# Optimization experiments

Measured on AMD Instinct MI355X. Metric: run time of the kernel, lower is better.

Reference implementation:

```python
import jax, jax.numpy as jnp
import numpy as np

B, L, D_MODEL = 2, 2048, 1024
D_STATE, D_CONV, EXPAND, DT_RANK = 16, 4, 2, 64
D_INNER = EXPAND * D_MODEL


def setup_inputs() -> dict:
    key = jax.random.key(0)
    ks = jax.random.split(key, 12)
    s = 0.02
    A_log = jnp.log(jnp.broadcast_to(jnp.arange(1, D_STATE + 1, dtype=jnp.float32), (D_INNER, D_STATE)))
    return {
        "x": jax.random.normal(ks[0], (B, L, D_MODEL), jnp.float32),
        "W_in": jax.random.normal(ks[1], (2 * D_INNER, D_MODEL), jnp.float32) * s,
        "conv_w": jax.random.normal(ks[2], (D_INNER, 1, D_CONV), jnp.float32) * 0.2,
        "conv_b": jax.random.normal(ks[3], (D_INNER,), jnp.float32) * s,
        "W_xp": jax.random.normal(ks[4], (DT_RANK + 2 * D_STATE, D_INNER), jnp.float32) * s,
        "W_dt": jax.random.normal(ks[5], (D_INNER, DT_RANK), jnp.float32) * 0.1,
        "b_dt": jax.random.uniform(ks[6], (D_INNER,), jnp.float32, -4.6, -2.3),  # ~softplus^-1 of small dt
        "A_log": A_log,
        "D": jnp.ones((D_INNER,), jnp.float32),
        "W_out_ssm": jax.random.normal(ks[7], (D_MODEL, D_INNER), jnp.float32) * s,
        "W_out": jax.random.normal(ks[8], (D_MODEL, D_MODEL), jnp.float32) * s,
        "b_out": jnp.zeros((D_MODEL,), jnp.float32),
    }


def _mamba_block(x, W_in, conv_w, conv_b, W_xp, W_dt, b_dt, A_log, D, W_out_ssm, W_out, b_out):
    d_inner = conv_b.shape[0]
    d_state = A_log.shape[1]
    dt_rank = W_dt.shape[1]
    d_conv = conv_w.shape[-1]

    # in_proj -> x branch and gate z
    xz = x @ W_in.T                         # [B, L, 2*d_inner]
    xin, z = jnp.split(xz, 2, axis=-1)

    # causal depthwise conv over time
    xc = jnp.transpose(xin, (0, 2, 1))      # [B, d_inner, L]
    xc = jax.lax.conv_general_dilated(
        xc, conv_w, window_strides=(1,), padding=[(d_conv - 1, 0)],
        feature_group_count=d_inner)
    xc = jax.nn.silu(xc + conv_b[None, :, None])
    xs = jnp.transpose(xc, (0, 2, 1))       # [B, L, d_inner]

    # input-dependent dt, B, C
    x_dbl = xs @ W_xp.T                     # [B, L, dt_rank + 2*d_state]
    dt, Bm, Cm = jnp.split(x_dbl, [dt_rank, dt_rank + d_state], axis=-1)
    dt = jax.nn.softplus(dt @ W_dt.T + b_dt)  # [B, L, d_inner]

    A = -jnp.exp(A_log)                     # [d_inner, d_state]

    def step(h, inp):
        dt_t, B_t, C_t, x_t = inp           # [B,di] [B,ds] [B,ds] [B,di]
        dA = jnp.exp(dt_t[:, :, None] * A)                      # [B, di, ds]
        h = h * dA + (dt_t * x_t)[:, :, None] * B_t[:, None, :]  # [B, di, ds]
        y = jnp.einsum('bds,bs->bd', h, C_t)
        return h, y

    h0 = jnp.zeros((x.shape[0], d_inner, d_state), x.dtype)
    tm = lambda a: jnp.swapaxes(a, 0, 1)    # time-major
    _, ys = jax.lax.scan(step, h0, (tm(dt), tm(Bm), tm(Cm), tm(xs)))
    y = jnp.swapaxes(ys, 0, 1)              # [B, L, d_inner]

    y = y + xs * D
    y = y * jax.nn.silu(z)
    y = y @ W_out_ssm.T                     # mamba-internal out_proj -> d_model
    return y @ W_out.T + b_out              # wrapper out_proj


def reference(x, W_in, conv_w, conv_b, W_xp, W_dt, b_dt, A_log, D, W_out_ssm, W_out, b_out):
    return _mamba_block(x, W_in, conv_w, conv_b, W_xp, W_dt, b_dt, A_log, D, W_out_ssm, W_out, b_out)
```

## Files before the change

### kernel.cpp

```cpp
#include <hip/hip_runtime.h>
#include <hip/hip_bf16.h>
#include <cmath>
#include <cstdint>

typedef __bf16 bf16_t;
typedef bf16_t bf16x8 __attribute__((ext_vector_type(8)));
typedef bf16_t bf16x4 __attribute__((ext_vector_type(4)));
typedef float f32x4 __attribute__((ext_vector_type(4)));

#define BB 2
#define LL 2048
#define DMODEL 1024
#define DINNER 2048
#define DSTATE 16
#define NC 64
#define CHUNK 32
#define KSEG 256

#define EXP2F(x) __builtin_amdgcn_exp2f(x)

#define CVT_N0 1048576
#define CVT_N1 2097152
#define CVT_N2 2129920
#define CVT_N3 2392064
__global__ void k_cvt_all(const float* __restrict__ x, const float* __restrict__ Win,
                          const float* __restrict__ Wdt, const float* __restrict__ Wo,
                          bf16_t* __restrict__ x_b, bf16_t* __restrict__ Win_b,
                          bf16_t* __restrict__ Wdt_b, bf16_t* __restrict__ Wo_b) {
    int i = blockIdx.x * 256 + threadIdx.x;
    if (i >= CVT_N3) return;
    const float* src; bf16_t* dst; int j;
    if (i < CVT_N0)      { src = x;   dst = x_b;   j = i; }
    else if (i < CVT_N1) { src = Win; dst = Win_b; j = i - CVT_N0; }
    else if (i < CVT_N2) { src = Wdt; dst = Wdt_b; j = i - CVT_N1; }
    else                 { src = Wo;  dst = Wo_b;  j = i - CVT_N2; }
    float4 v = reinterpret_cast<const float4*>(src)[j];
    bf16x4 o;
    o[0] = (bf16_t)v.x; o[1] = (bf16_t)v.y; o[2] = (bf16_t)v.z; o[3] = (bf16_t)v.w;
    reinterpret_cast<bf16x4*>(dst)[j] = o;
}

__global__ void k_cvt_wxp(const float* __restrict__ in, bf16_t* __restrict__ out) {
    int i = blockIdx.x * 256 + threadIdx.x;
    int r = i >> 11, c = i & (DINNER - 1);
    float v = (r < 96) ? in[r * DINNER + c] : 0.f;
    out[i] = (bf16_t)v;
}

__global__ __launch_bounds__(256) void k_cvt_wosT(const float* __restrict__ Wos,
                                                  bf16_t* __restrict__ WosT) {
    __shared__ float tile[64][65];
    const int tid = threadIdx.x;
    const int m0 = (blockIdx.x & 15) * 64;
    const int d0 = (blockIdx.x >> 4) * 64;
    const int dl = tid & 63;
    #pragma unroll 4
    for (int i = 0; i < 16; ++i) {
        const int mr = (tid >> 6) + i * 4;
        tile[dl][mr] = Wos[(size_t)(m0 + mr) * DINNER + d0 + dl];
    }
    __syncthreads();
    const int dr = tid >> 2;
    const int q  = tid & 3;
    bf16_t* op = WosT + (size_t)(d0 + dr) * DMODEL + m0 + q * 16;
    bf16x8 v0, v1;
    #pragma unroll
    for (int j = 0; j < 8; ++j) v0[j] = (bf16_t)tile[dr][q * 16 + j];
    #pragma unroll
    for (int j = 0; j < 8; ++j) v1[j] = (bf16_t)tile[dr][q * 16 + 8 + j];
    reinterpret_cast<bf16x8*>(op)[0] = v0;
    reinterpret_cast<bf16x8*>(op)[1] = v1;
}

__device__ __forceinline__ void gload16(const void* g, void* l) {
    __builtin_amdgcn_global_load_lds(
        (const __attribute__((address_space(1))) void*)g,
        (__attribute__((address_space(3))) void*)l,
        16, 0, 0);
}

__global__ __launch_bounds__(256) void k_gemm3(
    const bf16_t* __restrict__ x_b, const bf16_t* __restrict__ Win_b,
    const bf16_t* __restrict__ Wo_b, const bf16_t* __restrict__ WosT_b,
    bf16_t* __restrict__ Wc_b, bf16_t* __restrict__ xin_b,
    bf16_t* __restrict__ zsT) {
    __shared__ bf16_t sA[2][128 * 32];
    __shared__ bf16_t sB[2][128 * 32];
    const int tid = threadIdx.x;
    const int wid = tid >> 6, lane = tid & 63;

    const int bid = (blockIdx.x & 7) * 144 + (blockIdx.x >> 3);
    const bf16_t* A; const bf16_t* Bt; int N, tile, sub;
    if (bid < 128)      { sub = 0; A = Wo_b;  Bt = WosT_b; N = 2048; tile = bid; }
    else if (bid < 640) { sub = 1; A = x_b;   Bt = Win_b;  N = 2048; tile = bid - 128; }
    else                { sub = 2; A = Win_b + (size_t)DINNER * DMODEL; Bt = x_b; N = 4096; tile = bid - 640; }
    const int ntile = N >> 7;
    const int m0 = (tile / ntile) << 7;
    const int n0 = (tile % ntile) << 7;
    const int wr = wid >> 1, wc = wid & 1;
    f32x4 acc[4][4] = {};

    const bf16_t* ap = A + (size_t)(m0 + (tid >> 2)) * 1024 + (tid & 3) * 8;
    const bf16_t* bp = Bt + (size_t)(n0 + (tid >> 2)) * 1024 + (tid & 3) * 8;
    char* sA0 = (char*)sA[0] + wid * 1024;
    char* sB0 = (char*)sB[0] + wid * 1024;
    char* sA1 = (char*)sA[1] + wid * 1024;
    char* sB1 = (char*)sB[1] + wid * 1024;

    const int lm = lane & 15, lk = (lane >> 4) * 8;
    const bf16_t* rA0 = sA[0] + (wr * 64 + lm) * 32 + lk;
    const bf16_t* rB0 = sB[0] + (wc * 64 + lm) * 32 + lk;
    const bf16_t* rA1 = sA[1] + (wr * 64 + lm) * 32 + lk;
    const bf16_t* rB1 = sB[1] + (wc * 64 + lm) * 32 + lk;

    for (int kt = 0; kt < 1024; kt += 64) {
        __syncthreads();
        gload16(ap + kt, sA0);
        gload16(ap + kt + (size_t)64 * 1024, sA0 + 4096);
        gload16(bp + kt, sB0);
        gload16(bp + kt + (size_t)64 * 1024, sB0 + 4096);
        gload16(ap + kt + 32, sA1);
        gload16(ap + kt + 32 + (size_t)64 * 1024, sA1 + 4096);
        gload16(bp + kt + 32, sB1);
        gload16(bp + kt + 32 + (size_t)64 * 1024, sB1 + 4096);
        __syncthreads();
        {
            bf16x8 fa[4], fb[4];
            #pragma unroll
            for (int i = 0; i < 4; ++i) fa[i] = *(const bf16x8*)(rA0 + i * 16 * 32);
            #pragma unroll
            for (int j = 0; j < 4; ++j) fb[j] = *(const bf16x8*)(rB0 + j * 16 * 32);
            #pragma unroll
            for (int i = 0; i < 4; ++i)
                #pragma unroll
                for (int j = 0; j < 4; ++j)
                    acc[i][j] = __builtin_amdgcn_mfma_f32_16x16x32_bf16(fa[i], fb[j], acc[i][j], 0, 0, 0);
        }
        {
            bf16x8 fa[4], fb[4];
            #pragma unroll
            for (int i = 0; i < 4; ++i) fa[i] = *(const bf16x8*)(rA1 + i * 16 * 32);
            #pragma unroll
            for (int j = 0; j < 4; ++j) fb[j] = *(const bf16x8*)(rB1 + j * 16 * 32);
            #pragma unroll
            for (int i = 0; i < 4; ++i)
                #pragma unroll
                for (int j = 0; j < 4; ++j)
                    acc[i][j] = __builtin_amdgcn_mfma_f32_16x16x32_bf16(fa[i], fb[j], acc[i][j], 0, 0, 0);
        }
    }

    const int row0 = m0 + wr * 64 + (lane >> 4) * 4;
    const int col0 = n0 + wc * 64 + lm;
    #pragma unroll
    for (int i = 0; i < 4; ++i) {
        #pragma unroll
        for (int j = 0; j < 4; ++j) {
            #pragma unroll
            for (int r = 0; r < 4; ++r) {
                int row = row0 + i * 16 + r;
                int c = col0 + j * 16;
                float v = acc[i][j][r];
                if (sub == 0)      Wc_b[(size_t)row * DINNER + c] = (bf16_t)v;
                else if (sub == 1) xin_b[(size_t)row * DINNER + c] = (bf16_t)v;
                else               zsT[(size_t)row * (BB * LL) + c] = (bf16_t)(v / (1.f + __expf(-v)));
            }
        }
    }
}

enum { EPI_BF16 = 0, EPI_BIAS = 1, EPI_SOFTPLUS_RB = 3, EPI_PARTK = 4 };

template <int EPI>
__global__ void k_gemm_bt(const bf16_t* __restrict__ A, const bf16_t* __restrict__ Bt,
                          int M, int N, int Kloop, int lda, int ldb,
                          float* __restrict__ C, bf16_t* __restrict__ Cb,
                          const float* __restrict__ bias,
                          float* __restrict__ o_part) {
    __shared__ bf16_t sA[2][128 * 32];
    __shared__ bf16_t sB[2][128 * 32];
    const int tid = threadIdx.x;
    const int wid = tid >> 6, lane = tid & 63;
    const int bx = (blockIdx.x & 7) * ((int)gridDim.x >> 3) + (blockIdx.x >> 3);
    int m0, n0, k0 = 0, seg = 0;
    if (EPI == EPI_PARTK) {
        m0 = (bx & 31) << 7;
        n0 = 0;
        seg = bx >> 5;
        k0 = seg * KSEG;
    } else {
        const int ntile = N >> 7;
        m0 = (bx / ntile) << 7;
        n0 = (bx % ntile) << 7;
    }
    const int wr = wid >> 1, wc = wid & 1;
    f32x4 acc[4][4] = {};

    const bf16_t* ap = A + (size_t)(m0 + (tid >> 2)) * lda + (tid & 3) * 8 + k0;
    const bf16_t* bp = Bt + (size_t)(n0 + (tid >> 2)) * ldb + (tid & 3) * 8 + k0;
    char* sA0 = (char*)sA[0] + wid * 1024;
    char* sB0 = (char*)sB[0] + wid * 1024;
    char* sA1 = (char*)sA[1] + wid * 1024;
    char* sB1 = (char*)sB[1] + wid * 1024;

    const int lm = lane & 15, lk = (lane >> 4) * 8;
    const bf16_t* rA0 = sA[0] + (wr * 64 + lm) * 32 + lk;
    const bf16_t* rB0 = sB[0] + (wc * 64 + lm) * 32 + lk;
    const bf16_t* rA1 = sA[1] + (wr * 64 + lm) * 32 + lk;
    const bf16_t* rB1 = sB[1] + (wc * 64 + lm) * 32 + lk;

    for (int kt = 0; kt < Kloop; kt += 64) {
        __syncthreads();
        gload16(ap + kt, sA0);
        gload16(ap + kt + (size_t)64 * lda, sA0 + 4096);
        gload16(bp + kt, sB0);
        gload16(bp + kt + (size_t)64 * ldb, sB0 + 4096);
        gload16(ap + kt + 32, sA1);
        gload16(ap + kt + 32 + (size_t)64 * lda, sA1 + 4096);
        gload16(bp + kt + 32, sB1);
        gload16(bp + kt + 32 + (size_t)64 * ldb, sB1 + 4096);
        __syncthreads();
        {
            bf16x8 fa[4], fb[4];
            #pragma unroll
            for (int i = 0; i < 4; ++i) fa[i] = *(const bf16x8*)(rA0 + i * 16 * 32);
            #pragma unroll
            for (int j = 0; j < 4; ++j) fb[j] = *(const bf16x8*)(rB0 + j * 16 * 32);
            #pragma unroll
            for (int i = 0; i < 4; ++i)
                #pragma unroll
                for (int j = 0; j < 4; ++j)
                    acc[i][j] = __builtin_amdgcn_mfma_f32_16x16x32_bf16(fa[i], fb[j], acc[i][j], 0, 0, 0);
        }
        {
            bf16x8 fa[4], fb[4];
            #pragma unroll
            for (int i = 0; i < 4; ++i) fa[i] = *(const bf16x8*)(rA1 + i * 16 * 32);
            #pragma unroll
            for (int j = 0; j < 4; ++j) fb[j] = *(const bf16x8*)(rB1 + j * 16 * 32);
            #pragma unroll
            for (int i = 0; i < 4; ++i)
                #pragma unroll
                for (int j = 0; j < 4; ++j)
                    acc[i][j] = __builtin_amdgcn_mfma_f32_16x16x32_bf16(fa[i], fb[j], acc[i][j], 0, 0, 0);
        }
    }

    const int row0 = m0 + wr * 64 + (lane >> 4) * 4;
    const int col0 = n0 + wc * 64 + lm;
    float* Cp = (EPI == EPI_PARTK)
        ? o_part + (size_t)seg * ((size_t)4096 * 128)
        : C;
    #pragma unroll
    for (int i = 0; i < 4; ++i) {
        #pragma unroll
        for (int j = 0; j < 4; ++j) {
            #pragma unroll
            for (int r = 0; r < 4; ++r) {
                int row = row0 + i * 16 + r;
                int c = col0 + j * 16;
                float v = acc[i][j][r];
                if (EPI == EPI_BF16) {
                    Cb[(size_t)row * N + c] = (bf16_t)v;
                } else if (EPI == EPI_BIAS) {
                    C[(size_t)row * N + c] = v + bias[c];
                } else if (EPI == EPI_SOFTPLUS_RB) {
                    float xv = v + bias[row];
                    float sp = fmaxf(xv, 0.f) + log1pf(__expf(-fabsf(xv)));
                    Cb[(size_t)row * N + c] = (bf16_t)sp;
                } else {
                    Cp[(size_t)row * 128 + c] = v;
                }
            }
        }
    }
}

__global__ __launch_bounds__(256) void k_split_reduce(
    const float* __restrict__ part, bf16_t* __restrict__ dtr,
    float* __restrict__ Bmf, float* __restrict__ Cmf) {
    int idx = blockIdx.x * 256 + threadIdx.x;
    int row = idx >> 7, c = idx & 127;
    float s = 0.f;
    #pragma unroll
    for (int g = 0; g < 8; ++g) s += part[(size_t)g * (4096 * 128) + idx];
    if (c < 64) dtr[(size_t)row * 64 + c] = (bf16_t)s;
    else if (c < 80) Bmf[(size_t)row * 16 + (c - 64)] = s;
    else if (c < 96) Cmf[(size_t)row * 16 + (c - 80)] = s;
}

__global__ __launch_bounds__(256) void k_conv(
    const bf16_t* __restrict__ xin, const float* __restrict__ cw,
    const float* __restrict__ cb, bf16_t* __restrict__ xs_b,
    bf16_t* __restrict__ xsT) {
    __shared__ float tile[64][65];
    const int tid = threadIdx.x;
    const int d0  = (blockIdx.x & 31) * 64;
    const int bl0 = (blockIdx.x >> 5) * 64;
    const int dl = tid & 63;
    const int d  = d0 + dl;
    const float w0 = cw[d * 4], w1 = cw[d * 4 + 1], w2 = cw[d * 4 + 2], w3 = cw[d * 4 + 3];
    const float bias = cb[d];
    const int l0 = bl0 & (LL - 1);
    #pragma unroll 4
    for (int i = 0; i < 16; ++i) {
        const int blr = (tid >> 6) + i * 4;
        const int bl = bl0 + blr;
        const int l  = l0 + blr;
        const bf16_t* rp = xin + (size_t)bl * DINNER + d;
        float acc = fmaf(w3, (float)rp[0], bias);
        if (l >= 1) acc = fmaf(w2, (float)rp[-(int)DINNER], acc);
        if (l >= 2) acc = fmaf(w1, (float)rp[-2 * (int)DINNER], acc);
        if (l >= 3) acc = fmaf(w0, (float)rp[-3 * (int)DINNER], acc);
        float sv = acc / (1.f + __expf(-acc));
        xs_b[(size_t)bl * DINNER + d] = (bf16_t)sv;
        tile[dl][blr] = sv;
    }
    __syncthreads();
    const int dr = tid >> 2;
    const int q  = tid & 3;
    bf16_t* op = xsT + (size_t)(d0 + dr) * (BB * LL) + bl0 + q * 16;
    bf16x8 v0, v1;
    #pragma unroll
    for (int j = 0; j < 8; ++j) v0[j] = (bf16_t)tile[dr][q * 16 + j];
    #pragma unroll
    for (int j = 0; j < 8; ++j) v1[j] = (bf16_t)tile[dr][q * 16 + 8 + j];
    reinterpret_cast<bf16x8*>(op)[0] = v0;
    reinterpret_cast<bf16x8*>(op)[1] = v1;
}


__global__ __launch_bounds__(256) void k_scan_p1(
    const bf16_t* __restrict__ dtT, const bf16_t* __restrict__ xsT,
    const float* __restrict__ Bm, const float* __restrict__ A_log,
    float* __restrict__ alpha, float* __restrict__ beta) {
    __shared__ float sB[CHUNK * 16];
    const int db = blockIdx.x & 7;
    const int ck = (blockIdx.x >> 3) & (NC - 1);
    const int b  = blockIdx.x >> 9;
    const int tid = threadIdx.x;
    const int d  = db * 256 + tid;
    const int t0 = ck * CHUNK;

    const float* Bsrc = Bm + ((size_t)b * LL + t0) * 16;
    sB[tid] = Bsrc[tid];
    sB[tid + 256] = Bsrc[tid + 256];

    f32x4 a2[4];
    #pragma unroll
    for (int q = 0; q < 4; ++q) {
        f32x4 av = reinterpret_cast<const f32x4*>(A_log + d * 16)[q];
        #pragma unroll
        for (int j = 0; j < 4; ++j) a2[q][j] = -__expf(av[j]) * 1.44269504f;
    }
    const bf16x8* dtp = reinterpret_cast<const bf16x8*>(dtT + (size_t)d * (BB * LL) + b * LL + t0);
    const bf16x8* xsp = reinterpret_cast<const bf16x8*>(xsT + (size_t)d * (BB * LL) + b * LL + t0);

    bf16x8 dtl[4], xsl[4];
    #pragma unroll
    for (int q = 0; q < 4; ++q) dtl[q] = dtp[q];
    #pragma unroll
    for (int q = 0; q < 4; ++q) xsl[q] = xsp[q];

    __syncthreads();

    float al[16], be[16];
    #pragma unroll
    for (int s = 0; s < 16; ++s) { al[s] = 1.f; be[s] = 0.f; }

    #pragma unroll
    for (int t = 0; t < CHUNK; ++t) {
        float dtv = (float)dtl[t >> 3][t & 7];
        float xv  = (float)xsl[t >> 3][t & 7];
        float dtx = dtv * xv;
        #pragma unroll
        for (int q = 0; q < 4; ++q) {
            f32x4 Bq = *reinterpret_cast<const f32x4*>(sB + t * 16 + q * 4);
            #pragma unroll
            for (int j = 0; j < 4; ++j) {
                const int s = q * 4 + j;
                float dA = EXP2F(dtv * a2[q][j]);
                al[s] *= dA;
                be[s] = fmaf(be[s], dA, dtx * Bq[j]);
            }
        }
    }
    float* ap = alpha + ((size_t)(b * NC + ck)) * (DINNER * 16) + (size_t)d * 16;
    float* bp = beta  + ((size_t)(b * NC + ck)) * (DINNER * 16) + (size_t)d * 16;
    #pragma unroll
    for (int q = 0; q < 4; ++q) {
        f32x4 av, bv;
        #pragma unroll
        for (int j = 0; j < 4; ++j) { av[j] = al[q * 4 + j]; bv[j] = be[q * 4 + j]; }
        reinterpret_cast<f32x4*>(ap)[q] = av;
        reinterpret_cast<f32x4*>(bp)[q] = bv;
    }
}

__global__ __launch_bounds__(256) void k_scan_p2(
    const float* __restrict__ alpha, const float* __restrict__ beta,
    float* __restrict__ H) {
    const int gid = blockIdx.x * 256 + threadIdx.x;
    const int b = gid >> 15, r = gid & 32767;
    float h = 0.f;
    #pragma unroll 8
    for (int ck = 0; ck < NC; ++ck) {
        const size_t i = ((size_t)(b * NC + ck)) * 32768 + r;
        H[i] = h;
        h = fmaf(alpha[i], h, beta[i]);
    }
}

__global__ __launch_bounds__(256) void k_scan_p3(
    const bf16_t* __restrict__ dtT, const bf16_t* __restrict__ xsT,
    const float* __restrict__ Bm, const float* __restrict__ Cm,
    const bf16_t* __restrict__ zsT, const float* __restrict__ A_log,
    const float* __restrict__ Dp, const float* __restrict__ H,
    bf16_t* __restrict__ y) {
    __shared__ float sB[CHUNK * 16];
    __shared__ float sC[CHUNK * 16];
    const int db = blockIdx.x & 7;
    const int ck = (blockIdx.x >> 3) & (NC - 1);
    const int b  = blockIdx.x >> 9;
    const int tid = threadIdx.x;
    const int d  = db * 256 + tid;
    const int t0 = ck * CHUNK;

    const float* Bsrc = Bm + ((size_t)b * LL + t0) * 16;
    const float* Csrc = Cm + ((size_t)b * LL + t0) * 16;
    sB[tid] = Bsrc[tid];
    sB[tid + 256] = Bsrc[tid + 256];
    sC[tid] = Csrc[tid];
    sC[tid + 256] = Csrc[tid + 256];

    f32x4 a2[4];
    #pragma unroll
    for (int q = 0; q < 4; ++q) {
        f32x4 av = reinterpret_cast<const f32x4*>(A_log + d * 16)[q];
        #pragma unroll
        for (int j = 0; j < 4; ++j) a2[q][j] = -__expf(av[j]) * 1.44269504f;
    }
    const float Dd = Dp[d];
    const bf16x8* dtp = reinterpret_cast<const bf16x8*>(dtT + (size_t)d * (BB * LL) + b * LL + t0);
    const bf16x8* xsp = reinterpret_cast<const bf16x8*>(xsT + (size_t)d * (BB * LL) + b * LL + t0);
    const bf16x8* zp  = reinterpret_cast<const bf16x8*>(zsT + (size_t)d * (BB * LL) + b * LL + t0);
    bf16_t* yp = y + ((size_t)b * LL + t0) * DINNER + d;

    bf16x8 dtl[4], xsl[4], zsl[4];
    #pragma unroll
    for (int q = 0; q < 4; ++q) dtl[q] = dtp[q];
    #pragma unroll
    for (int q = 0; q < 4; ++q) xsl[q] = xsp[q];
    #pragma unroll
    for (int q = 0; q < 4; ++q) zsl[q] = zp[q];

    float h[16];
    {
        const f32x4* hp = reinterpret_cast<const f32x4*>(H + ((size_t)(b * NC + ck)) * 32768 + (size_t)d * 16);
        #pragma unroll
        for (int q = 0; q < 4; ++q) {
            f32x4 hv = hp[q];
            #pragma unroll
            for (int j = 0; j < 4; ++j) h[q * 4 + j] = hv[j];
        }
    }

    __syncthreads();

    #pragma unroll
    for (int t = 0; t < CHUNK; ++t) {
        float dtv = (float)dtl[t >> 3][t & 7];
        float xv  = (float)xsl[t >> 3][t & 7];
        float zv  = (float)zsl[t >> 3][t & 7];
        float dtx = dtv * xv;
        float yacc = 0.f;
        #pragma unroll
        for (int q = 0; q < 4; ++q) {
            f32x4 Bq = *reinterpret_cast<const f32x4*>(sB + t * 16 + q * 4);
            f32x4 Cq = *reinterpret_cast<const f32x4*>(sC + t * 16 + q * 4);
            #pragma unroll
            for (int j = 0; j < 4; ++j) {
                const int s = q * 4 + j;
                float dA = EXP2F(dtv * a2[q][j]);
                h[s] = fmaf(h[s], dA, dtx * Bq[j]);
                yacc = fmaf(h[s], Cq[j], yacc);
            }
        }
        float yv = (yacc + xv * Dd) * zv;
        yp[(size_t)t * DINNER] = (bf16_t)yv;
    }
}

extern "C" void kernel_launch(void* const* d_in, const int* in_sizes, int n_in,
                              void* d_out, int out_size, void* d_ws, size_t ws_size,
                              hipStream_t stream) {
    const float* x      = (const float*)d_in[0];
    const float* W_in   = (const float*)d_in[1];
    const float* conv_w = (const float*)d_in[2];
    const float* conv_b = (const float*)d_in[3];
    const float* W_xp   = (const float*)d_in[4];
    const float* W_dt   = (const float*)d_in[5];
    const float* b_dt   = (const float*)d_in[6];
    const float* A_log  = (const float*)d_in[7];
    const float* Dvec   = (const float*)d_in[8];
    const float* W_os   = (const float*)d_in[9];
    const float* W_o    = (const float*)d_in[10];
    const float* b_o    = (const float*)d_in[11];
    float* out = (float*)d_out;

    char* base = (char*)d_ws;
    size_t off = 0;
    auto alloc = [&](size_t bytes) -> char* {
        char* p = base + off;
        off += (bytes + 255) & ~(size_t)255;
        return p;
    };
    const int MR = BB * LL;
    bf16_t* x_b   = (bf16_t*)alloc((size_t)MR * DMODEL * 2);
    bf16_t* Win_b = (bf16_t*)alloc((size_t)4096 * 1024 * 2);
    bf16_t* xin_b = (bf16_t*)alloc((size_t)MR * DINNER * 2);
    bf16_t* xs_b  = (bf16_t*)alloc((size_t)MR * DINNER * 2);
    bf16_t* zsT   = (bf16_t*)alloc((size_t)DINNER * MR * 2);
    bf16_t* xsT   = (bf16_t*)alloc((size_t)DINNER * MR * 2);
    bf16_t* dtT_b = (bf16_t*)alloc((size_t)DINNER * MR * 2);
    float*  Hbuf  = (float*)alloc((size_t)BB * NC * DINNER * 16 * 4);
    bf16_t* y_b   = (bf16_t*)alloc((size_t)MR * DINNER * 2);
    bf16_t* dtr_b = (bf16_t*)alloc((size_t)MR * 64 * 2);
    float*  Bmf   = (float*)alloc((size_t)MR * 16 * 4);
    float*  Cmf   = (float*)alloc((size_t)MR * 16 * 4);
    bf16_t* Wxp_b = (bf16_t*)alloc((size_t)128 * DINNER * 2);
    bf16_t* Wdt_b = (bf16_t*)alloc((size_t)DINNER * 64 * 2);
    bf16_t* WosT_b= (bf16_t*)alloc((size_t)DINNER * DMODEL * 2);
    bf16_t* Wo_b  = (bf16_t*)alloc((size_t)DMODEL * DMODEL * 2);
    bf16_t* Wc_b  = (bf16_t*)alloc((size_t)DMODEL * DINNER * 2);

    float* alphab = (float*)xin_b;
    float* betab  = (float*)x_b;
    float* partk  = Hbuf;

    k_cvt_all<<<CVT_N3 / 256, 256, 0, stream>>>(
        x, W_in, W_dt, W_o, x_b, Win_b, Wdt_b, Wo_b);
    k_cvt_wxp<<<(128 * DINNER) / 256, 256, 0, stream>>>(W_xp, Wxp_b);
    k_cvt_wosT<<<16 * 32, 256, 0, stream>>>(W_os, WosT_b);

    k_gemm3<<<1152, 256, 0, stream>>>(
        x_b, Win_b, Wo_b, WosT_b, Wc_b, xin_b, zsT);
    k_conv<<<(MR / 64) * (DINNER / 64), 256, 0, stream>>>(xin_b, conv_w, conv_b, xs_b, xsT);
    k_gemm_bt<EPI_PARTK><<<8 * 32, 256, 0, stream>>>(
        xs_b, Wxp_b, MR, 128, KSEG, DINNER, DINNER,
        nullptr, nullptr, nullptr, partk);
    k_split_reduce<<<(MR * 128) / 256, 256, 0, stream>>>(partk, dtr_b, Bmf, Cmf);
    k_gemm_bt<EPI_SOFTPLUS_RB><<<(DINNER / 128) * (MR / 128), 256, 0, stream>>>(
        Wdt_b, dtr_b, DINNER, MR, 64, 64, 64,
        nullptr, dtT_b, b_dt, nullptr);
    k_scan_p1<<<BB * NC * (DINNER / 256), 256, 0, stream>>>(dtT_b, xsT, Bmf, A_log, alphab, betab);
    k_scan_p2<<<(BB * DINNER * DSTATE) / 256, 256, 0, stream>>>(alphab, betab, Hbuf);
    k_scan_p3<<<BB * NC * (DINNER / 256), 256, 0, stream>>>(dtT_b, xsT, Bmf, Cmf, zsT, A_log, Dvec, Hbuf, y_b);
    k_gemm_bt<EPI_BIAS><<<(MR / 128) * (DMODEL / 128), 256, 0, stream>>>(
        y_b, Wc_b, MR, DMODEL, DINNER, DINNER, DINNER,
        out, nullptr, b_o, nullptr);
}
```

Measured before the change: 253.2 us.

## Software-pipeline GEMM K-loop with double buffering and merge conversion kernels

The GEMM main loops (k_gemm3 and k_gemm_bt) switch from loading two 32-wide K slices and then waiting at a barrier to a double-buffered pipeline. Each iteration prefetches the next slice into the alternate LDS buffer while MFMAs run on the current one, and the MFMA block is wrapped in s_setprio. This should hide global-to-LDS latency behind compute, at the cost of a barrier every 32 K instead of two per 64 K. Separately, the three fp32-to-bf16 weight conversion kernels are merged into one launch to cut launch overhead.

```diff
diff --git a/kernel.cpp b/kernel.cpp
--- a/kernel.cpp
+++ b/kernel.cpp
@@ -23,53 +23,56 @@
 #define CVT_N1 2097152
 #define CVT_N2 2129920
 #define CVT_N3 2392064
-__global__ void k_cvt_all(const float* __restrict__ x, const float* __restrict__ Win,
-                          const float* __restrict__ Wdt, const float* __restrict__ Wo,
-                          bf16_t* __restrict__ x_b, bf16_t* __restrict__ Win_b,
-                          bf16_t* __restrict__ Wdt_b, bf16_t* __restrict__ Wo_b) {
-    int i = blockIdx.x * 256 + threadIdx.x;
-    if (i >= CVT_N3) return;
-    const float* src; bf16_t* dst; int j;
-    if (i < CVT_N0)      { src = x;   dst = x_b;   j = i; }
-    else if (i < CVT_N1) { src = Win; dst = Win_b; j = i - CVT_N0; }
-    else if (i < CVT_N2) { src = Wdt; dst = Wdt_b; j = i - CVT_N1; }
-    else                 { src = Wo;  dst = Wo_b;  j = i - CVT_N2; }
-    float4 v = reinterpret_cast<const float4*>(src)[j];
-    bf16x4 o;
-    o[0] = (bf16_t)v.x; o[1] = (bf16_t)v.y; o[2] = (bf16_t)v.z; o[3] = (bf16_t)v.w;
-    reinterpret_cast<bf16x4*>(dst)[j] = o;
-}
-
-__global__ void k_cvt_wxp(const float* __restrict__ in, bf16_t* __restrict__ out) {
-    int i = blockIdx.x * 256 + threadIdx.x;
-    int r = i >> 11, c = i & (DINNER - 1);
-    float v = (r < 96) ? in[r * DINNER + c] : 0.f;
-    out[i] = (bf16_t)v;
-}
-
-__global__ __launch_bounds__(256) void k_cvt_wosT(const float* __restrict__ Wos,
-                                                  bf16_t* __restrict__ WosT) {
-    __shared__ float tile[64][65];
+#define CVT_NB0 9344
+#define CVT_NB1 10368
+#define CVT_NBT 10880
+__global__ __launch_bounds__(256) void k_cvt_all(
+    const float* __restrict__ x, const float* __restrict__ Win,
+    const float* __restrict__ Wdt, const float* __restrict__ Wo,
+    const float* __restrict__ Wxp, const float* __restrict__ Wos,
+    bf16_t* __restrict__ x_b, bf16_t* __restrict__ Win_b,
+    bf16_t* __restrict__ Wdt_b, bf16_t* __restrict__ Wo_b,
+    bf16_t* __restrict__ Wxp_b, bf16_t* __restrict__ WosT_b) {
     const int tid = threadIdx.x;
-    const int m0 = (blockIdx.x & 15) * 64;
-    const int d0 = (blockIdx.x >> 4) * 64;
-    const int dl = tid & 63;
-    #pragma unroll 4
-    for (int i = 0; i < 16; ++i) {
-        const int mr = (tid >> 6) + i * 4;
-        tile[dl][mr] = Wos[(size_t)(m0 + mr) * DINNER + d0 + dl];
-    }
-    __syncthreads();
-    const int dr = tid >> 2;
-    const int q  = tid & 3;
-    bf16_t* op = WosT + (size_t)(d0 + dr) * DMODEL + m0 + q * 16;
-    bf16x8 v0, v1;
-    #pragma unroll
-    for (int j = 0; j < 8; ++j) v0[j] = (bf16_t)tile[dr][q * 16 + j];
-    #pragma unroll
-    for (int j = 0; j < 8; ++j) v1[j] = (bf16_t)tile[dr][q * 16 + 8 + j];
-    reinterpret_cast<bf16x8*>(op)[0] = v0;
-    reinterpret_cast<bf16x8*>(op)[1] = v1;
+    if (blockIdx.x < CVT_NB0) {
+        int i = blockIdx.x * 256 + tid;
+        const float* src; bf16_t* dst; int j;
+        if (i < CVT_N0)      { src = x;   dst = x_b;   j = i; }
+        else if (i < CVT_N1) { src = Win; dst = Win_b; j = i - CVT_N0; }
+        else if (i < CVT_N2) { src = Wdt; dst = Wdt_b; j = i - CVT_N1; }
+        else                 { src = Wo;  dst = Wo_b;  j = i - CVT_N2; }
+        float4 v = reinterpret_cast<const float4*>(src)[j];
+        bf16x4 o;
+        o[0] = (bf16_t)v.x; o[1] = (bf16_t)v.y; o[2] = (bf16_t)v.z; o[3] = (bf16_t)v.w;
+        reinterpret_cast<bf16x4*>(dst)[j] = o;
+    } else if (blockIdx.x < CVT_NB1) {
+        int i = (blockIdx.x - CVT_NB0) * 256 + tid;
+        int r = i >> 11, c = i & (DINNER - 1);
+        float v = (r < 96) ? Wxp[r * DINNER + c] : 0.f;
+        Wxp_b[i] = (bf16_t)v;
+    } else {
+        __shared__ float tile[64][65];
+        const int bid = blockIdx.x - CVT_NB1;
+        const int m0 = (bid & 15) * 64;
+        const int d0 = (bid >> 4) * 64;
+        const int dl = tid & 63;
+        #pragma unroll 4
+        for (int i = 0; i < 16; ++i) {
+            const int mr = (tid >> 6) + i * 4;
+            tile[dl][mr] = Wos[(size_t)(m0 + mr) * DINNER + d0 + dl];
+        }
+        __syncthreads();
+        const int dr = tid >> 2;
+        const int q  = tid & 3;
+        bf16_t* op = WosT_b + (size_t)(d0 + dr) * DMODEL + m0 + q * 16;
+        bf16x8 v0, v1;
+        #pragma unroll
+        for (int j = 0; j < 8; ++j) v0[j] = (bf16_t)tile[dr][q * 16 + j];
+        #pragma unroll
+        for (int j = 0; j < 8; ++j) v1[j] = (bf16_t)tile[dr][q * 16 + 8 + j];
+        reinterpret_cast<bf16x8*>(op)[0] = v0;
+        reinterpret_cast<bf16x8*>(op)[1] = v1;
+    }
 }
 
 __device__ __forceinline__ void gload16(const void* g, void* l) {
@@ -102,52 +105,38 @@
 
     const bf16_t* ap = A + (size_t)(m0 + (tid >> 2)) * 1024 + (tid & 3) * 8;
     const bf16_t* bp = Bt + (size_t)(n0 + (tid >> 2)) * 1024 + (tid & 3) * 8;
-    char* sA0 = (char*)sA[0] + wid * 1024;
-    char* sB0 = (char*)sB[0] + wid * 1024;
-    char* sA1 = (char*)sA[1] + wid * 1024;
-    char* sB1 = (char*)sB[1] + wid * 1024;
-
     const int lm = lane & 15, lk = (lane >> 4) * 8;
-    const bf16_t* rA0 = sA[0] + (wr * 64 + lm) * 32 + lk;
-    const bf16_t* rB0 = sB[0] + (wc * 64 + lm) * 32 + lk;
-    const bf16_t* rA1 = sA[1] + (wr * 64 + lm) * 32 + lk;
-    const bf16_t* rB1 = sB[1] + (wc * 64 + lm) * 32 + lk;
-
-    for (int kt = 0; kt < 1024; kt += 64) {
+
+    auto stage = [&](int buf, int kt) {
+        char* dA = (char*)sA[buf] + wid * 1024;
+        char* dB = (char*)sB[buf] + wid * 1024;
+        gload16(ap + kt, dA);
+        gload16(ap + kt + (size_t)64 * 1024, dA + 4096);
+        gload16(bp + kt, dB);
+        gload16(bp + kt + (size_t)64 * 1024, dB + 4096);
+    };
+
+    stage(0, 0);
+    __syncthreads();
+    int cur = 0;
+    for (int kt = 0; kt < 1024; kt += 32) {
+        if (kt + 32 < 1024) stage(cur ^ 1, kt + 32);
+        const bf16_t* rA = sA[cur] + (wr * 64 + lm) * 32 + lk;
+        const bf16_t* rB = sB[cur] + (wc * 64 + lm) * 32 + lk;
+        bf16x8 fa[4], fb[4];
+        #pragma unroll
+        for (int i = 0; i < 4; ++i) fa[i] = *(const bf16x8*)(rA + i * 16 * 32);
+        #pragma unroll
+        for (int j = 0; j < 4; ++j) fb[j] = *(const bf16x8*)(rB + j * 16 * 32);
+        __builtin_amdgcn_s_setprio(1);
+        #pragma unroll
+        for (int i = 0; i < 4; ++i)
+            #pragma unroll
+            for (int j = 0; j < 4; ++j)
+                acc[i][j] = __builtin_amdgcn_mfma_f32_16x16x32_bf16(fa[i], fb[j], acc[i][j], 0, 0, 0);
+        __builtin_amdgcn_s_setprio(0);
         __syncthreads();
-        gload16(ap + kt, sA0);
-        gload16(ap + kt + (size_t)64 * 1024, sA0 + 4096);
-        gload16(bp + kt, sB0);
-        gload16(bp + kt + (size_t)64 * 1024, sB0 + 4096);
-        gload16(ap + kt + 32, sA1);
-        gload16(ap + kt + 32 + (size_t)64 * 1024, sA1 + 4096);
-        gload16(bp + kt + 32, sB1);
-        gload16(bp + kt + 32 + (size_t)64 * 1024, sB1 + 4096);
-        __syncthreads();
-        {
-            bf16x8 fa[4], fb[4];
-            #pragma unroll
-            for (int i = 0; i < 4; ++i) fa[i] = *(const bf16x8*)(rA0 + i * 16 * 32);
-            #pragma unroll
-            for (int j = 0; j < 4; ++j) fb[j] = *(const bf16x8*)(rB0 + j * 16 * 32);
-            #pragma unroll
-            for (int i = 0; i < 4; ++i)
-                #pragma unroll
-                for (int j = 0; j < 4; ++j)
-                    acc[i][j] = __builtin_amdgcn_mfma_f32_16x16x32_bf16(fa[i], fb[j], acc[i][j], 0, 0, 0);
-        }
-        {
-            bf16x8 fa[4], fb[4];
-            #pragma unroll
-            for (int i = 0; i < 4; ++i) fa[i] = *(const bf16x8*)(rA1 + i * 16 * 32);
-            #pragma unroll
-            for (int j = 0; j < 4; ++j) fb[j] = *(const bf16x8*)(rB1 + j * 16 * 32);
-            #pragma unroll
-            for (int i = 0; i < 4; ++i)
-                #pragma unroll
-                for (int j = 0; j < 4; ++j)
-                    acc[i][j] = __builtin_amdgcn_mfma_f32_16x16x32_bf16(fa[i], fb[j], acc[i][j], 0, 0, 0);
-        }
+        cur ^= 1;
     }
 
     const int row0 = m0 + wr * 64 + (lane >> 4) * 4;
@@ -172,11 +161,12 @@
 enum { EPI_BF16 = 0, EPI_BIAS = 1, EPI_SOFTPLUS_RB = 3, EPI_PARTK = 4 };
 
 template <int EPI>
-__global__ void k_gemm_bt(const bf16_t* __restrict__ A, const bf16_t* __restrict__ Bt,
-                          int M, int N, int Kloop, int lda, int ldb,
-                          float* __restrict__ C, bf16_t* __restrict__ Cb,
-                          const float* __restrict__ bias,
-                          float* __restrict__ o_part) {
+__global__ __launch_bounds__(256) void k_gemm_bt(
+    const bf16_t* __restrict__ A, const bf16_t* __restrict__ Bt,
+    int M, int N, int Kloop, int lda, int ldb,
+    float* __restrict__ C, bf16_t* __restrict__ Cb,
+    const float* __restrict__ bias,
+    float* __restrict__ o_part) {
     __shared__ bf16_t sA[2][128 * 32];
     __shared__ bf16_t sB[2][128 * 32];
     const int tid = threadIdx.x;
@@ -198,52 +188,38 @@
 
     const bf16_t* ap = A + (size_t)(m0 + (tid >> 2)) * lda + (tid & 3) * 8 + k0;
     const bf16_t* bp = Bt + (size_t)(n0 + (tid >> 2)) * ldb + (tid & 3) * 8 + k0;
-    char* sA0 = (char*)sA[0] + wid * 1024;
-    char* sB0 = (char*)sB[0] + wid * 1024;
-    char* sA1 = (char*)sA[1] + wid * 1024;
-    char* sB1 = (char*)sB[1] + wid * 1024;
-
     const int lm = lane & 15, lk = (lane >> 4) * 8;
-    const bf16_t* rA0 = sA[0] + (wr * 64 + lm) * 32 + lk;
-    const bf16_t* rB0 = sB[0] + (wc * 64 + lm) * 32 + lk;
-    const bf16_t* rA1 = sA[1] + (wr * 64 + lm) * 32 + lk;
-    const bf16_t* rB1 = sB[1] + (wc * 64 + lm) * 32 + lk;
-
-    for (int kt = 0; kt < Kloop; kt += 64) {
+
+    auto stage = [&](int buf, int kt) {
+        char* dA = (char*)sA[buf] + wid * 1024;
+        char* dB = (char*)sB[buf] + wid * 1024;
+        gload16(ap + kt, dA);
+        gload16(ap + kt + (size_t)64 * lda, dA + 4096);
+        gload16(bp + kt, dB);
+        gload16(bp + kt + (size_t)64 * ldb, dB + 4096);
+    };
+
+    stage(0, 0);
+    __syncthreads();
+    int cur = 0;
+    for (int kt = 0; kt < Kloop; kt += 32) {
+        if (kt + 32 < Kloop) stage(cur ^ 1, kt + 32);
+        const bf16_t* rA = sA[cur] + (wr * 64 + lm) * 32 + lk;
+        const bf16_t* rB = sB[cur] + (wc * 64 + lm) * 32 + lk;
+        bf16x8 fa[4], fb[4];
+        #pragma unroll
+        for (int i = 0; i < 4; ++i) fa[i] = *(const bf16x8*)(rA + i * 16 * 32);
+        #pragma unroll
+        for (int j = 0; j < 4; ++j) fb[j] = *(const bf16x8*)(rB + j * 16 * 32);
+        __builtin_amdgcn_s_setprio(1);
+        #pragma unroll
+        for (int i = 0; i < 4; ++i)
+            #pragma unroll
+            for (int j = 0; j < 4; ++j)
+                acc[i][j] = __builtin_amdgcn_mfma_f32_16x16x32_bf16(fa[i], fb[j], acc[i][j], 0, 0, 0);
+        __builtin_amdgcn_s_setprio(0);
         __syncthreads();
-        gload16(ap + kt, sA0);
-        gload16(ap + kt + (size_t)64 * lda, sA0 + 4096);
-        gload16(bp + kt, sB0);
-        gload16(bp + kt + (size_t)64 * ldb, sB0 + 4096);
-        gload16(ap + kt + 32, sA1);
-        gload16(ap + kt + 32 + (size_t)64 * lda, sA1 + 4096);
-        gload16(bp + kt + 32, sB1);
-        gload16(bp + kt + 32 + (size_t)64 * ldb, sB1 + 4096);
-        __syncthreads();
-        {
-            bf16x8 fa[4], fb[4];
-            #pragma unroll
-            for (int i = 0; i < 4; ++i) fa[i] = *(const bf16x8*)(rA0 + i * 16 * 32);
-            #pragma unroll
-            for (int j = 0; j < 4; ++j) fb[j] = *(const bf16x8*)(rB0 + j * 16 * 32);
-            #pragma unroll
-            for (int i = 0; i < 4; ++i)
-                #pragma unroll
-                for (int j = 0; j < 4; ++j)
-                    acc[i][j] = __builtin_amdgcn_mfma_f32_16x16x32_bf16(fa[i], fb[j], acc[i][j], 0, 0, 0);
-        }
-        {
-            bf16x8 fa[4], fb[4];
-            #pragma unroll
-            for (int i = 0; i < 4; ++i) fa[i] = *(const bf16x8*)(rA1 + i * 16 * 32);
-            #pragma unroll
-            for (int j = 0; j < 4; ++j) fb[j] = *(const bf16x8*)(rB1 + j * 16 * 32);
-            #pragma unroll
-            for (int i = 0; i < 4; ++i)
-                #pragma unroll
-                for (int j = 0; j < 4; ++j)
-                    acc[i][j] = __builtin_amdgcn_mfma_f32_16x16x32_bf16(fa[i], fb[j], acc[i][j], 0, 0, 0);
-        }
+        cur ^= 1;
     }
 
     const int row0 = m0 + wr * 64 + (lane >> 4) * 4;
@@ -538,10 +514,9 @@
     float* betab  = (float*)x_b;
     float* partk  = Hbuf;
 
-    k_cvt_all<<<CVT_N3 / 256, 256, 0, stream>>>(
-        x, W_in, W_dt, W_o, x_b, Win_b, Wdt_b, Wo_b);
-    k_cvt_wxp<<<(128 * DINNER) / 256, 256, 0, stream>>>(W_xp, Wxp_b);
-    k_cvt_wosT<<<16 * 32, 256, 0, stream>>>(W_os, WosT_b);
+    k_cvt_all<<<CVT_NBT, 256, 0, stream>>>(
+        x, W_in, W_dt, W_o, W_xp, W_os,
+        x_b, Win_b, Wdt_b, Wo_b, Wxp_b, WosT_b);
 
     k_gemm3<<<1152, 256, 0, stream>>>(
         x_b, Win_b, Wo_b, WosT_b, Wc_b, xin_b, zsT);
```

Result: faster. 245.5 us (-3.0%).
